# Performance work log

Measured on AMD Instinct MI355X. Metric: run time of the kernel, lower is better.

## Reference

```python
import jax, jax.numpy as jnp
import numpy as np

B, S, D, H = 8, 512, 1024, 16
DH = D // H
GAMMA = 0.1      # kl_gamma
KL_EPS = 1e-10
LN_EPS = 1e-5
SCALE = 1.0 / np.sqrt(DH).astype(np.float32)


def setup_inputs() -> dict:
    key = jax.random.key(0)
    ks = iter(jax.random.split(key, 32))
    rnd = lambda shape, s: jax.random.normal(next(ks), shape, jnp.float32) * s
    inp = {
        'title_features': rnd((B, S, D), 1.0),
        'content_features': rnd((B, S, D), 1.0),
    }
    for pre in ('t2c', 'c2t'):
        # small Q/K weights + bias 1.0 keep row-means of scores positive (log is defined)
        inp[pre + '_wq'] = rnd((D, D), 0.02); inp[pre + '_bq'] = jnp.ones((D,), jnp.float32)
        inp[pre + '_wk'] = rnd((D, D), 0.02); inp[pre + '_bk'] = jnp.ones((D,), jnp.float32)
        inp[pre + '_wv'] = rnd((D, D), 0.02); inp[pre + '_bv'] = jnp.zeros((D,), jnp.float32)
        inp[pre + '_wo'] = rnd((D, D), 0.02); inp[pre + '_bo'] = jnp.zeros((D,), jnp.float32)
    inp['gate_w'] = rnd((2 * D, D), 0.02)
    inp['gate_b'] = jnp.zeros((D,), jnp.float32)
    inp['ln_g'] = jnp.ones((D,), jnp.float32)
    inp['ln_b'] = jnpps = jnp.zeros((D,), jnp.float32)
    inp['ln_b'] = jnp.zeros((D,), jnp.float32)
    return inp


def _daa(q_in, k_in, v_in, wq, bq, wk, bk, wv, bv, wo, bo):
    """DivergenceAlignedAttention forward (eval mode, use_uniform_target=False)."""
    Bq, Sq, _ = q_in.shape
    Sk = k_in.shape[1]
    Q = (q_in @ wq + bq).reshape(Bq, Sq, H, DH)
    K = (k_in @ wk + bk).reshape(Bq, Sk, H, DH)
    V = (v_in @ wv + bv).reshape(Bq, Sk, H, DH)
    scores = jnp.einsum('bqhd,bkhd->bhqk', Q, K) * SCALE           # [B,H,Sq,Sk]
    tgt = jnp.mean(scores, axis=-1, keepdims=True)                 # row mean
    scores = scores + GAMMA * jnp.log(tgt + KL_EPS)                # fused KL term
    attn = jax.nn.softmax(scores, axis=-1)
    ctx = jnp.einsum('bhqk,bkhd->bqhd', attn, V).reshape(Bq, Sq, D)
    return ctx @ wo + bo


def _layer_norm(x, g, b):
    mu = jnp.mean(x, axis=-1, keepdims=True)
    var = jnp.mean(jnp.square(x - mu), axis=-1, keepdims=True)
    return g * (x - mu) / jnp.sqrt(var + LN_EPS) + b


def reference(title_features, content_features,
              t2c_wq, t2c_bq, t2c_wk, t2c_bk, t2c_wv, t2c_bv, t2c_wo, t2c_bo,
              c2t_wq, c2t_bq, c2t_wk, c2t_bk, c2t_wv, c2t_bv, c2t_wo, c2t_bo,
              gate_w, gate_b, ln_g, ln_b):
    t2c = _daa(content_features, title_features, title_features,
               t2c_wq, t2c_bq, t2c_wk, t2c_bk, t2c_wv, t2c_bv, t2c_wo, t2c_bo)
    c2t = _daa(title_features, content_features, content_features,
               c2t_wq, c2t_bq, c2t_wk, c2t_bk, c2t_wv, c2t_bv, c2t_wo, c2t_bo)
    gate_t = jax.nn.sigmoid(jnp.concatenate([title_features, t2c], axis=-1) @ gate_w + gate_b)
    gate_c = jax.nn.sigmoid(jnp.concatenate([content_features, c2t], axis=-1) @ gate_w + gate_b)
    fused_title = _layer_norm(gate_t * title_features + (1.0 - gate_t) * t2c, ln_g, ln_b)
    fused_content = _layer_norm(gate_c * content_features + (1.0 - gate_c) * c2t, ln_g, ln_b)
    return (fused_title, fused_content)
```

## Files before the change

### kernel.cpp

```cpp
#include <hip/hip_runtime.h>
#include <cstdint>
#include <cstddef>

typedef unsigned short ushort_t;
typedef unsigned int u32;
typedef __attribute__((ext_vector_type(8))) short bf16x8;
typedef __attribute__((ext_vector_type(4))) float f32x4;
typedef __attribute__((ext_vector_type(4))) unsigned short u16x4;

#define DEV static __device__ __forceinline__

DEV ushort_t f2bf(float f) {
  u32 x = __float_as_uint(f);
  x += 0x7fff + ((x >> 16) & 1);
  return (ushort_t)(x >> 16);
}
DEV float bf2f(ushort_t u) { return __uint_as_float(((u32)u) << 16); }

DEV void gload16(const ushort_t* g, ushort_t* l) {
  __builtin_amdgcn_global_load_lds(
      (const __attribute__((address_space(1))) void*)g,
      (__attribute__((address_space(3))) void*)l, 16, 0, 0);
}

#define VMW(n) asm volatile("s_waitcnt vmcnt(" #n ")" ::: "memory")
#define LGKM0 asm volatile("s_waitcnt lgkmcnt(0)" ::: "memory")
#define BAR() __builtin_amdgcn_s_barrier()


__global__ __launch_bounds__(256) void cvt_inputs(
    const float* __restrict__ xa, const float* __restrict__ xb,
    ushort_t* __restrict__ oa, ushort_t* __restrict__ ob) {
  int i = blockIdx.x * 256 + threadIdx.x;
  f32x4 va = ((const f32x4*)xa)[i];
  f32x4 vb = ((const f32x4*)xb)[i];
  u16x4 ua, ub;
#pragma unroll
  for (int j = 0; j < 4; ++j) { ua[j] = f2bf(va[j]); ub[j] = f2bf(vb[j]); }
  ((u16x4*)oa)[i] = ua;
  ((u16x4*)ob)[i] = ub;
}

struct Src11 { const float* p[11]; };

__global__ __launch_bounds__(256) void transpose_cvt(
    Src11 srcs, ushort_t* __restrict__ WTall, ushort_t* __restrict__ WgT,
    ushort_t* __restrict__ WoBF) {
  const int z = blockIdx.z;
  if (z != 8 && blockIdx.y >= 32) return;
  const float* src = srcs.p[z];
  int tx = threadIdx.x & 31, ty = threadIdx.x >> 5;
  int n0 = blockIdx.x << 5, k0 = blockIdx.y << 5;
  if (z >= 9) {
    ushort_t* dst = WoBF + ((size_t)(z - 9) << 20);
#pragma unroll
    for (int i = 0; i < 4; ++i) {
      size_t off = (size_t)(k0 + ty + i * 8) * 1024 + n0 + tx;
      dst[off] = f2bf(src[off]);
    }
    return;
  }
  const int K = (z == 8) ? 2048 : 1024;
  ushort_t* dst = (z == 8) ? WgT : WTall + ((size_t)z << 20);
  __shared__ float t[32][33];
#pragma unroll
  for (int i = 0; i < 4; ++i)
    t[ty + i * 8][tx] = src[(size_t)(k0 + ty + i * 8) * 1024 + n0 + tx];
  __syncthreads();
#pragma unroll
  for (int i = 0; i < 4; ++i)
    dst[(size_t)(n0 + ty + i * 8) * K + k0 + tx] = f2bf(t[tx][ty + i * 8]);
}

__global__ __launch_bounds__(256) void gb2_kernel(
    const float* __restrict__ bo0, const float* __restrict__ bo1,
    const ushort_t* __restrict__ WgT, float* __restrict__ gb2) {
  int idx = blockIdx.x * 256 + threadIdx.x;
  int dir = idx >> 10, n = idx & 1023;
  const float* bo = dir ? bo1 : bo0;
  const ushort_t* wrow = WgT + ((size_t)n << 11) + 1024;
  float s = 0.f;
  for (int k = 0; k < 1024; ++k) s += bo[k] * bf2f(wrow[k]);
  gb2[idx] = s;
}

__global__ __launch_bounds__(256, 3) void gemm_wp(
    const ushort_t* __restrict__ WgT, const ushort_t* __restrict__ WoBF,
    ushort_t* __restrict__ WpT) {
  __shared__ ushort_t As[128 * 64];
  __shared__ ushort_t Bs[128 * 64];
  const int tid = threadIdx.x;
  const int w = tid >> 6, lane = tid & 63;
  const int g = lane >> 4, c = lane & 15;
  const int wm = (w >> 1) << 6, wn = (w & 1) << 6;
  const int m0 = blockIdx.x << 7, n0 = blockIdx.y << 7;
  const int group = m0 >> 10;
  const int csw = (lane & 7) ^ (lane >> 3);

  f32x4 acc[4][4];
#pragma unroll
  for (int i = 0; i < 4; ++i)
#pragma unroll
    for (int j = 0; j < 4; ++j) acc[i][j] = f32x4{0.f, 0.f, 0.f, 0.f};

  for (int k0 = 0; k0 < 1024; k0 += 64) {
#pragma unroll
    for (int i = 0; i < 4; ++i) {
      const int chunk = (w << 2) + i;
      const int row = (chunk << 3) + (lane >> 3);
      gload16(WgT + ((size_t)((m0 + row) & 1023) << 11) + 1024 + k0 + (csw << 3),
              &As[(size_t)chunk << 9]);
      gload16(WoBF + ((size_t)group << 20) + ((size_t)(n0 + row) << 10) + k0 + (csw << 3),
              &Bs[(size_t)chunk << 9]);
    }
    __syncthreads();
    const int cg = c & 7;
#pragma unroll
    for (int ks = 0; ks < 2; ++ks) {
      bf16x8 af[4], bfr[4];
#pragma unroll
      for (int mi = 0; mi < 4; ++mi)
        af[mi] = *(const bf16x8*)&As[((wm + mi * 16 + c) << 6) +
                                     ((((ks << 2) | g) ^ cg) << 3)];
#pragma unroll
      for (int ni = 0; ni < 4; ++ni)
        bfr[ni] = *(const bf16x8*)&Bs[((wn + ni * 16 + c) << 6) +
                                      ((((ks << 2) | g) ^ cg) << 3)];
#pragma unroll
      for (int mi = 0; mi < 4; ++mi)
#pragma unroll
        for (int ni = 0; ni < 4; ++ni)
          acc[mi][ni] = __builtin_amdgcn_mfma_f32_16x16x32_bf16(
              af[mi], bfr[ni], acc[mi][ni], 0, 0, 0);
    }
    __syncthreads();
  }
#pragma unroll
  for (int ni = 0; ni < 4; ++ni) {
    const int n = n0 + wn + ni * 16 + c;
#pragma unroll
    for (int mi = 0; mi < 4; ++mi) {
      const int mb = m0 + wm + mi * 16 + (g << 2);
      f32x4 a = acc[mi][ni];
#pragma unroll
      for (int r = 0; r < 4; ++r)
        WpT[((size_t)group << 20) + ((size_t)((mb + r) & 1023) << 10) + n] = f2bf(a[r]);
    }
  }
}

enum { G_QKV = 0, G_OG = 1 };
struct Bias8 { const float* p[8]; };

#define RD_A(Q)                                                                \
  _Pragma("unroll") for (int m2 = 0; m2 < 2; ++m2)                             \
    _Pragma("unroll") for (int kk = 0; kk < 2; ++kk)                           \
      af[m2][kk] = *(const bf16x8*)&As[buf][(((wm << 7) + (((Q)*2 + m2) << 4) + c) << 6) + \
                                           ((((kk << 2) | g) ^ c7) << 3)]
#define MM(Q)                                                                  \
  _Pragma("unroll") for (int m2 = 0; m2 < 2; ++m2)                             \
    _Pragma("unroll") for (int nf = 0; nf < 4; ++nf) {                         \
      acc[(Q)*2 + m2][nf] = __builtin_amdgcn_mfma_f32_16x16x32_bf16(           \
          af[m2][0], bfr[nf][0], acc[(Q)*2 + m2][nf], 0, 0, 0);                \
      acc[(Q)*2 + m2][nf] = __builtin_amdgcn_mfma_f32_16x16x32_bf16(           \
          af[m2][1], bfr[nf][1], acc[(Q)*2 + m2][nf], 0, 0, 0);                \
    }

#define GTILE(T_, ST_, V0_, V1_, V2_, V3_)                                     \
  do {                                                                         \
    const int buf = (T_)&1;                                                    \
    const int ko = ((T_) + 1) << 6;                                            \
    bf16x8 af[2][2];                                                           \
    VMW(V0_); BAR();                                                           \
    _Pragma("unroll") for (int nf = 0; nf < 4; ++nf)                           \
      _Pragma("unroll") for (int kk = 0; kk < 2; ++kk)                         \
        bfr[nf][kk] = *(const bf16x8*)&Bs[buf][(((wn << 6) + (nf << 4) + c) << 6) + \
                                              ((((kk << 2) | g) ^ c7) << 3)];  \
    RD_A(0);                                                                   \
    if (ST_) stageB(buf ^ 1, ko, 0);                                           \
    BAR(); LGKM0;                                                              \
    __builtin_amdgcn_s_setprio(1); MM(0); __builtin_amdgcn_s_setprio(0);       \
    VMW(V1_); BAR();                                                           \
    RD_A(1);                                                                   \
    if (ST_) stageB(buf ^ 1, ko, 1);                                           \
    BAR(); LGKM0;                                                              \
    __builtin_amdgcn_s_setprio(1); MM(1); __builtin_amdgcn_s_setprio(0);       \
    VMW(V2_); BAR();                                                           \
    RD_A(2);                                                                   \
    if (ST_) { stageA(buf ^ 1, ko, 0); stageA(buf ^ 1, ko, 1); }               \
    BAR(); LGKM0;                                                              \
    __builtin_amdgcn_s_setprio(1); MM(2); __builtin_amdgcn_s_setprio(0);       \
    VMW(V3_); BAR();                                                           \
    RD_A(3);                                                                   \
    if (ST_) { stageA(buf ^ 1, ko, 2); stageA(buf ^ 1, ko, 3); }               \
    BAR(); LGKM0;                                                              \
    __builtin_amdgcn_s_setprio(1); MM(3); __builtin_amdgcn_s_setprio(0);       \
  } while (0)

template <int MODE>
__global__ __launch_bounds__(512, 2) void gemm256(
    const ushort_t* __restrict__ Aa, const ushort_t* __restrict__ Ab,
    const ushort_t* __restrict__ WTall, const ushort_t* __restrict__ WgT,
    const ushort_t* __restrict__ WpT, Bias8 bt,
    ushort_t* __restrict__ outQ, ushort_t* __restrict__ gl) {
  __shared__ ushort_t As[2][16384];
  __shared__ ushort_t Bs[2][16384];
  const int tid = threadIdx.x;
  const int wid = tid >> 6, lane = tid & 63;
  const int g = lane >> 4, c = lane & 15, c7 = c & 7;
  const int wm = wid >> 2, wn = wid & 3;
  constexpr int NB = (MODE == G_QKV) ? 512 : 256;
  const int bid = (int)blockIdx.x;
  const int wk = (bid & 7) * (NB >> 3) + (bid >> 3);
  const int mt = wk & 31, nt = wk >> 5;
  const int m0 = mt << 8, n0 = nt << 8;
  const int group = m0 >> 12;
  const int nch = n0 >> 10;

  const ushort_t* Asrc = (MODE == G_QKV)
      ? (group ? Ab : Aa) + ((size_t)(m0 & 4095) << 10)
      : Aa + ((size_t)m0 << 10);

  const ushort_t* Bbase;
  int bstride, bidx = -1;
  if (MODE == G_QKV) {
    if (nch < 3) {
      bidx = group * 3 + nch;
      Bbase = WTall + ((size_t)bidx << 20) + ((size_t)(n0 & 1023) << 10);
      bstride = 1024;
    } else {
      Bbase = WgT + ((size_t)(n0 & 1023) << 11);
      bstride = 2048;
    }
  } else {
    if (nch == 0) {
      Bbase = WTall + ((size_t)(6 + group) << 20) + ((size_t)n0 << 10);
      bstride = 1024;
    } else {
      Bbase = WpT + ((size_t)group << 20) + ((size_t)(n0 & 1023) << 10);
      bstride = 1024;
    }
  }

  auto stageB = [&](int bf_, int ko, int h) {
#pragma unroll
    for (int i = 0; i < 2; ++i) {
      int rl = (i << 6) + (wid << 3) + (lane >> 3);
      int row = (h << 7) + rl;
      int cs = (lane & 7) ^ (lane >> 3);
      gload16(Bbase + (size_t)row * bstride + ko + (cs << 3),
              &Bs[bf_][(h << 13) + (i << 12) + (wid << 9)]);
    }
  };
  auto stageA = [&](int bf_, int ko, int q) {
    int rl = (wid << 3) + (lane >> 3);
    int row = (q << 5) + (rl & 31) + ((rl & 32) << 2);
    int cs = (lane & 7) ^ (lane >> 3);
    gload16(Asrc + ((size_t)row << 10) + ko + (cs << 3),
            &As[bf_][((q << 5) + ((wid & 3) << 3) + ((wid >> 2) << 7)) << 6]);
  };

  f32x4 acc[8][4];
#pragma unroll
  for (int i = 0; i < 8; ++i)
#pragma unroll
    for (int j = 0; j < 4; ++j) acc[i][j] = f32x4{0.f, 0.f, 0.f, 0.f};

  stageB(0, 0, 0); stageB(0, 0, 1);
  stageA(0, 0, 0); stageA(0, 0, 1); stageA(0, 0, 2); stageA(0, 0, 3);

  bf16x8 bfr[4][2];
  for (int t = 0; t < 15; ++t) GTILE(t, 1, 3, 4, 5, 6);
  GTILE(15, 0, 3, 2, 1, 0);

  const float* bp_ = (MODE == G_QKV) ? (nch < 3 ? bt.p[bidx] : bt.p[6])
                                     : (nch == 0 ? bt.p[group] : bt.p[2 + group]);
#pragma unroll
  for (int mf = 0; mf < 8; ++mf) {
    const int mb = m0 + (wm << 7) + (mf << 4) + (g << 2);
#pragma unroll
    for (int nf = 0; nf < 4; ++nf) {
      const int n = n0 + (wn << 6) + (nf << 4) + c;
      const int nloc = n & 1023;
      const float bv = bp_[nloc];
      f32x4 a = acc[mf][nf];
      if (MODE == G_QKV) {
        if (nch < 3) {
          const int mrow = mb & 4095, b = mrow >> 9, s = mrow & 511;
          const int h = nloc >> 6, d = nloc & 63;
          ushort_t* base = outQ + ((size_t)bidx << 22);
          if (bidx == 1 || bidx == 5) {
            u16x4 o;
#pragma unroll
            for (int r = 0; r < 4; ++r) o[r] = f2bf(a[r] + bv);
            *(u16x4*)&base[(((size_t)((b * 16 + h) * 64 + d)) << 9) + s] = o;
          } else {
#pragma unroll
            for (int r = 0; r < 4; ++r)
              base[(((size_t)((b * 16 + h) * 512 + s + r)) << 6) + d] = f2bf(a[r] + bv);
          }
        } else {
#pragma unroll
          for (int r = 0; r < 4; ++r)
            gl[((size_t)(mb + r) << 10) + nloc] = f2bf(a[r] + bv);
        }
      } else {
        if (nch == 0) {
#pragma unroll
          for (int r = 0; r < 4; ++r)
            outQ[((size_t)(mb + r) << 10) + nloc] = f2bf(a[r] + bv);
        } else {
#pragma unroll
          for (int r = 0; r < 4; ++r) {
            size_t off = ((size_t)(mb + r) << 10) + nloc;
            gl[off] = f2bf(a[r] + bv + bf2f(gl[off]));
          }
        }
      }
    }
  }
}

__global__ __launch_bounds__(256, 2) void attn_kernel(
    const ushort_t* __restrict__ QKV, ushort_t* __restrict__ ctx) {
  __shared__ ushort_t kv[2][8192];
  const int tid = threadIdx.x, w = tid >> 6, lane = tid & 63;
  const int g = lane >> 4, c = lane & 15, c7 = c & 7;
  const int bid = (int)blockIdx.x;
  const int wid = (bid & 7) * 256 + (bid >> 3);
  const int dir = wid >> 10;
  const int bh = (wid >> 3) & 127, qt = wid & 7;
  const int q0 = (qt << 6) + (w << 4);
  const int qs = dir ? 2 : 3, ks = dir ? 4 : 0, vs = dir ? 5 : 1;
  const ushort_t* Qb = QKV + ((size_t)qs << 22) + ((size_t)bh << 15);
  const ushort_t* Kb = QKV + ((size_t)ks << 22) + ((size_t)bh << 15);
  const ushort_t* Vb = QKV + ((size_t)vs << 22) + ((size_t)bh << 15);

  auto stageK = [&](int b, int kc) {
#pragma unroll
    for (int i = 0; i < 4; ++i) {
      int idx = tid + (i << 8);
      int r = idx >> 3, sl = idx & 7;
      int cs = sl ^ (r & 7);
      gload16(Kb + (((size_t)((kc << 7) + r)) << 6) + (cs << 3), &kv[b][idx << 3]);
    }
  };
  auto stageV = [&](int b, int vc) {
#pragma unroll
    for (int i = 0; i < 4; ++i) {
      int idx = tid + (i << 8);
      int r = idx >> 4, sl = idx & 15;
      int cs = sl ^ (r & 15);
      gload16(Vb + ((size_t)r << 9) + (vc << 7) + (cs << 3), &kv[b][idx << 3]);
    }
  };

  bf16x8 qf0 = *(const bf16x8*)&Qb[((q0 + c) << 6) + (g << 3)];
  bf16x8 qf1 = *(const bf16x8*)&Qb[((q0 + c) << 6) + 32 + (g << 3)];

  f32x4 s[32];
  float mx = -1e30f;
  int buf = 0;
  stageK(0, 0);
  __syncthreads();
#pragma unroll
  for (int kc = 0; kc < 4; ++kc) {
    if (kc < 3) stageK(buf ^ 1, kc + 1);
    __builtin_amdgcn_s_setprio(1);
#pragma unroll
    for (int t = 0; t < 8; ++t) {
      const ushort_t* base = &kv[buf][((t << 4) + c) << 6];
      bf16x8 a0 = *(const bf16x8*)&base[(g ^ c7) << 3];
      bf16x8 a1 = *(const bf16x8*)&base[((4 | g) ^ c7) << 3];
      f32x4 z = {0.f, 0.f, 0.f, 0.f};
      z = __builtin_amdgcn_mfma_f32_16x16x32_bf16(a0, qf0, z, 0, 0, 0);
      z = __builtin_amdgcn_mfma_f32_16x16x32_bf16(a1, qf1, z, 0, 0, 0);
      s[kc * 8 + t] = z;
      mx = fmaxf(mx, fmaxf(fmaxf(z[0], z[1]), fmaxf(z[2], z[3])));
    }
    __builtin_amdgcn_s_setprio(0);
    __syncthreads();
    buf ^= 1;
  }
  stageV(0, 0);
  buf = 0;

  mx = fmaxf(mx, __shfl_xor(mx, 16, 64));
  mx = fmaxf(mx, __shfl_xor(mx, 32, 64));
  const float SC = 0.125f;
  float sum = 0.f;
#pragma unroll
  for (int t = 0; t < 32; ++t) {
#pragma unroll
    for (int r = 0; r < 4; ++r) {
      float p = __expf((s[t][r] - mx) * SC);
      s[t][r] = p;
      sum += p;
    }
  }
  sum += __shfl_xor(sum, 16, 64);
  sum += __shfl_xor(sum, 32, 64);
  const float inv = 1.0f / sum;

  f32x4 pacc[4];
#pragma unroll
  for (int dt = 0; dt < 4; ++dt) pacc[dt] = f32x4{0.f, 0.f, 0.f, 0.f};
  const int s1 = ((g & 1) << 5) + c;
  const int s2 = s1 + 16;
  const bool hi = (g >> 1) != 0;
  __syncthreads();
#pragma unroll
  for (int vc = 0; vc < 4; ++vc) {
    if (vc < 3) stageV(buf ^ 1, vc + 1);
#pragma unroll
    for (int t2l = 0; t2l < 4; ++t2l) {
      const int t2 = (vc << 2) + t2l;
      u32 A0 = ((u32)f2bf(s[2 * t2][1]) << 16) | f2bf(s[2 * t2][0]);
      u32 A1p = ((u32)f2bf(s[2 * t2][3]) << 16) | f2bf(s[2 * t2][2]);
      u32 B0 = ((u32)f2bf(s[2 * t2 + 1][1]) << 16) | f2bf(s[2 * t2 + 1][0]);
      u32 B1 = ((u32)f2bf(s[2 * t2 + 1][3]) << 16) | f2bf(s[2 * t2 + 1][2]);
      u32 xA0 = (u32)__shfl((int)A0, s1, 64), xA1 = (u32)__shfl((int)A1p, s1, 64);
      u32 xB0 = (u32)__shfl((int)B0, s1, 64), xB1 = (u32)__shfl((int)B1, s1, 64);
      u32 yA0 = (u32)__shfl((int)A0, s2, 64), yA1 = (u32)__shfl((int)A1p, s2, 64);
      u32 yB0 = (u32)__shfl((int)B0, s2, 64), yB1 = (u32)__shfl((int)B1, s2, 64);
      union { bf16x8 v; u32 wd[4]; } pb;
      pb.wd[0] = hi ? xB0 : xA0;
      pb.wd[1] = hi ? xB1 : xA1;
      pb.wd[2] = hi ? yB0 : yA0;
      pb.wd[3] = hi ? yB1 : yA1;
      __builtin_amdgcn_s_setprio(1);
#pragma unroll
      for (int dt = 0; dt < 4; ++dt) {
        bf16x8 av = *(const bf16x8*)
            &kv[buf][(((dt << 4) + c) << 7) + ((((t2l << 2) | g) ^ c) << 3)];
        pacc[dt] = __builtin_amdgcn_mfma_f32_16x16x32_bf16(av, pb.v, pacc[dt], 0, 0, 0);
      }
      __builtin_amdgcn_s_setprio(0);
    }
    __syncthreads();
    buf ^= 1;
  }

  const int b = bh >> 4, h = bh & 15;
  size_t obase = ((size_t)dir << 22) + ((size_t)(b * 512 + q0 + c) << 10) + (h << 6);
#pragma unroll
  for (int dt = 0; dt < 4; ++dt) {
    u16x4 o;
#pragma unroll
    for (int r = 0; r < 4; ++r) o[r] = f2bf(pacc[dt][r] * inv);
    *(u16x4*)&ctx[obase + (dt << 4) + (g << 2)] = o;
  }
}

__global__ __launch_bounds__(256) void fuse_ln(
    const float* __restrict__ xt, const float* __restrict__ xc,
    const ushort_t* __restrict__ ao, const ushort_t* __restrict__ gl,
    const float* __restrict__ lng, const float* __restrict__ lnb,
    float* __restrict__ out) {
  const int row = blockIdx.x, dir = row >> 12, r = row & 4095;
  const float* x = (dir ? xc : xt) + ((size_t)r << 10);
  const ushort_t* a = ao + ((size_t)row << 10);
  const ushort_t* glr = gl + ((size_t)row << 10);
  float* o = out + ((size_t)row << 10);
  const int t = threadIdx.x, w = t >> 6, lane = t & 63;
  f32x4 xv = ((const f32x4*)x)[t];
  u16x4 av = ((const u16x4*)a)[t];
  u16x4 gv = ((const u16x4*)glr)[t];
  f32x4 f;
  float sm = 0.f, sq = 0.f;
#pragma unroll
  for (int j = 0; j < 4; ++j) {
    float gate = 1.f / (1.f + __expf(-bf2f(gv[j])));
    float fv = gate * xv[j] + (1.f - gate) * bf2f(av[j]);
    f[j] = fv; sm += fv; sq += fv * fv;
  }
#pragma unroll
  for (int d = 1; d < 64; d <<= 1) {
    sm += __shfl_xor(sm, d, 64);
    sq += __shfl_xor(sq, d, 64);
  }
  __shared__ float ps[8];
  if (lane == 0) { ps[w] = sm; ps[4 + w] = sq; }
  __syncthreads();
  sm = ps[0] + ps[1] + ps[2] + ps[3];
  sq = ps[4] + ps[5] + ps[6] + ps[7];
  const float mu = sm * (1.f / 1024.f);
  const float var = sq * (1.f / 1024.f) - mu * mu;
  const float rstd = rsqrtf(var + 1e-5f);
  f32x4 lg = ((const f32x4*)lng)[t], lb = ((const f32x4*)lnb)[t];
  f32x4 ov;
#pragma unroll
  for (int j = 0; j < 4; ++j) ov[j] = lg[j] * (f[j] - mu) * rstd + lb[j];
  ((f32x4*)o)[t] = ov;
}

extern "C" void kernel_launch(void* const* d_in, const int* in_sizes, int n_in,
                              void* d_out, int out_size, void* d_ws, size_t ws_size,
                              hipStream_t stream) {
  (void)in_sizes; (void)n_in; (void)out_size; (void)ws_size;
  const float* title = (const float*)d_in[0];
  const float* content = (const float*)d_in[1];

  char* ws = (char*)d_ws;
  const size_t MB = 1u << 20;
  ushort_t* Xt    = (ushort_t*)(ws + 0 * MB);
  ushort_t* Xc    = (ushort_t*)(ws + 8 * MB);
  ushort_t* ctx   = (ushort_t*)(ws + 0 * MB);
  ushort_t* WTall = (ushort_t*)(ws + 16 * MB);
  ushort_t* WgT   = (ushort_t*)(ws + 32 * MB);
  ushort_t* QKV   = (ushort_t*)(ws + 36 * MB);
  ushort_t* ao    = (ushort_t*)(ws + 36 * MB);
  ushort_t* gl    = (ushort_t*)(ws + 84 * MB);
  ushort_t* WoBF  = (ushort_t*)(ws + 100 * MB);
  ushort_t* WpT   = (ushort_t*)(ws + 104 * MB);
  float*    gb2   = (float*)   (ws + 108 * MB);

  cvt_inputs<<<4096, 256, 0, stream>>>(title, content, Xt, Xc);

  Src11 srcs;
  srcs.p[0] = (const float*)d_in[4];  srcs.p[1] = (const float*)d_in[6];
  srcs.p[2] = (const float*)d_in[10]; srcs.p[3] = (const float*)d_in[2];
  srcs.p[4] = (const float*)d_in[12]; srcs.p[5] = (const float*)d_in[14];
  srcs.p[6] = (const float*)d_in[8];  srcs.p[7] = (const float*)d_in[16];
  srcs.p[8] = (const float*)d_in[18];
  srcs.p[9] = (const float*)d_in[8];  srcs.p[10] = (const float*)d_in[16];
  transpose_cvt<<<dim3(32, 64, 11), 256, 0, stream>>>(srcs, WTall, WgT, WoBF);

  gb2_kernel<<<8, 256, 0, stream>>>((const float*)d_in[9], (const float*)d_in[17],
                                    WgT, gb2);
  gemm_wp<<<dim3(16, 8), 256, 0, stream>>>(WgT, WoBF, WpT);

  Bias8 bq;
  bq.p[0] = (const float*)d_in[5];  bq.p[1] = (const float*)d_in[7];
  bq.p[2] = (const float*)d_in[11]; bq.p[3] = (const float*)d_in[3];
  bq.p[4] = (const float*)d_in[13]; bq.p[5] = (const float*)d_in[15];
  bq.p[6] = (const float*)d_in[19]; bq.p[7] = nullptr;
  gemm256<G_QKV><<<512, 512, 0, stream>>>(Xt, Xc, WTall, WgT, WpT, bq, QKV, gl);

  attn_kernel<<<2048, 256, 0, stream>>>(QKV, ctx);

  Bias8 bo;
  bo.p[0] = (const float*)d_in[9]; bo.p[1] = (const float*)d_in[17];
  bo.p[2] = gb2; bo.p[3] = gb2 + 1024;
  for (int i = 4; i < 8; ++i) bo.p[i] = nullptr;
  gemm256<G_OG><<<256, 512, 0, stream>>>(ctx, nullptr, WTall, WgT, WpT, bo, ao, gl);

  fuse_ln<<<8192, 256, 0, stream>>>(title, content, ao, gl,
                                    (const float*)d_in[20], (const float*)d_in[21],
                                    (float*)d_out);
}
```

Baseline: 253.2 us.

## Replace 256x256 pipelined GEMM with simpler 128x128 tiles and split gate partials

Swaps the 512-thread, 256x256-tile, double-buffered GEMM with a 256-thread, 128x128-tile, single-buffered kernel that runs more blocks per CU. The gate projection no longer does a read-modify-write on a shared buffer: the QKV pass writes the title/content gate part (with its bias and folded bo term) and the output pass writes its partial to a separate buffer. fuse_ln then sums the two partials before the sigmoid. The gb2 bias kernel also moves from one thread per output to one wave per output with a shuffle reduction. The trade is more tiles and no software pipelining inside the GEMM in exchange for higher occupancy and no read-after-write on gl, at the cost of one extra buffer read in fuse_ln.

```diff
diff --git a/kernel.cpp b/kernel.cpp
--- a/kernel.cpp
+++ b/kernel.cpp
@@ -22,10 +22,6 @@
       (const __attribute__((address_space(1))) void*)g,
       (__attribute__((address_space(3))) void*)l, 16, 0, 0);
 }
-
-#define VMW(n) asm volatile("s_waitcnt vmcnt(" #n ")" ::: "memory")
-#define LGKM0 asm volatile("s_waitcnt lgkmcnt(0)" ::: "memory")
-#define BAR() __builtin_amdgcn_s_barrier()
 
 
 __global__ __launch_bounds__(256) void cvt_inputs(
@@ -75,13 +71,17 @@
 __global__ __launch_bounds__(256) void gb2_kernel(
     const float* __restrict__ bo0, const float* __restrict__ bo1,
     const ushort_t* __restrict__ WgT, float* __restrict__ gb2) {
-  int idx = blockIdx.x * 256 + threadIdx.x;
-  int dir = idx >> 10, n = idx & 1023;
+  const int wgl = blockIdx.x * 4 + (threadIdx.x >> 6);
+  const int lane = threadIdx.x & 63;
+  const int dir = wgl >> 10, n = wgl & 1023;
   const float* bo = dir ? bo1 : bo0;
-  const ushort_t* wrow = WgT + ((size_t)n << 11) + 1024;
+  const ushort_t* wrow = WgT + ((size_t)n << 11) + 1024 + (lane << 4);
   float s = 0.f;
-  for (int k = 0; k < 1024; ++k) s += bo[k] * bf2f(wrow[k]);
-  gb2[idx] = s;
+#pragma unroll
+  for (int j = 0; j < 16; ++j) s += bo[(lane << 4) + j] * bf2f(wrow[j]);
+#pragma unroll
+  for (int d = 1; d < 64; d <<= 1) s += __shfl_xor(s, d, 64);
+  if (lane == 0) gb2[wgl] = s;
 }
 
 __global__ __launch_bounds__(256, 3) void gemm_wp(
@@ -149,142 +149,106 @@
   }
 }
 
-enum { G_QKV = 0, G_OG = 1 };
+enum { M_QKVG = 0, M_OG = 1 };
 struct Bias8 { const float* p[8]; };
 
-#define RD_A(Q)                                                                \
-  _Pragma("unroll") for (int m2 = 0; m2 < 2; ++m2)                             \
-    _Pragma("unroll") for (int kk = 0; kk < 2; ++kk)                           \
-      af[m2][kk] = *(const bf16x8*)&As[buf][(((wm << 7) + (((Q)*2 + m2) << 4) + c) << 6) + \
-                                           ((((kk << 2) | g) ^ c7) << 3)]
-#define MM(Q)                                                                  \
-  _Pragma("unroll") for (int m2 = 0; m2 < 2; ++m2)                             \
-    _Pragma("unroll") for (int nf = 0; nf < 4; ++nf) {                         \
-      acc[(Q)*2 + m2][nf] = __builtin_amdgcn_mfma_f32_16x16x32_bf16(           \
-          af[m2][0], bfr[nf][0], acc[(Q)*2 + m2][nf], 0, 0, 0);                \
-      acc[(Q)*2 + m2][nf] = __builtin_amdgcn_mfma_f32_16x16x32_bf16(           \
-          af[m2][1], bfr[nf][1], acc[(Q)*2 + m2][nf], 0, 0, 0);                \
-    }
-
-#define GTILE(T_, ST_, V0_, V1_, V2_, V3_)                                     \
-  do {                                                                         \
-    const int buf = (T_)&1;                                                    \
-    const int ko = ((T_) + 1) << 6;                                            \
-    bf16x8 af[2][2];                                                           \
-    VMW(V0_); BAR();                                                           \
-    _Pragma("unroll") for (int nf = 0; nf < 4; ++nf)                           \
-      _Pragma("unroll") for (int kk = 0; kk < 2; ++kk)                         \
-        bfr[nf][kk] = *(const bf16x8*)&Bs[buf][(((wn << 6) + (nf << 4) + c) << 6) + \
-                                              ((((kk << 2) | g) ^ c7) << 3)];  \
-    RD_A(0);                                                                   \
-    if (ST_) stageB(buf ^ 1, ko, 0);                                           \
-    BAR(); LGKM0;                                                              \
-    __builtin_amdgcn_s_setprio(1); MM(0); __builtin_amdgcn_s_setprio(0);       \
-    VMW(V1_); BAR();                                                           \
-    RD_A(1);                                                                   \
-    if (ST_) stageB(buf ^ 1, ko, 1);                                           \
-    BAR(); LGKM0;                                                              \
-    __builtin_amdgcn_s_setprio(1); MM(1); __builtin_amdgcn_s_setprio(0);       \
-    VMW(V2_); BAR();                                                           \
-    RD_A(2);                                                                   \
-    if (ST_) { stageA(buf ^ 1, ko, 0); stageA(buf ^ 1, ko, 1); }               \
-    BAR(); LGKM0;                                                              \
-    __builtin_amdgcn_s_setprio(1); MM(2); __builtin_amdgcn_s_setprio(0);       \
-    VMW(V3_); BAR();                                                           \
-    RD_A(3);                                                                   \
-    if (ST_) { stageA(buf ^ 1, ko, 2); stageA(buf ^ 1, ko, 3); }               \
-    BAR(); LGKM0;                                                              \
-    __builtin_amdgcn_s_setprio(1); MM(3); __builtin_amdgcn_s_setprio(0);       \
-  } while (0)
-
 template <int MODE>
-__global__ __launch_bounds__(512, 2) void gemm256(
+__global__ __launch_bounds__(256, 3) void gemm_kernel(
     const ushort_t* __restrict__ Aa, const ushort_t* __restrict__ Ab,
     const ushort_t* __restrict__ WTall, const ushort_t* __restrict__ WgT,
-    const ushort_t* __restrict__ WpT, Bias8 bt,
-    ushort_t* __restrict__ outQ, ushort_t* __restrict__ gl) {
-  __shared__ ushort_t As[2][16384];
-  __shared__ ushort_t Bs[2][16384];
+    const ushort_t* __restrict__ WpT, Bias8 bt, const float* __restrict__ gb2,
+    ushort_t* __restrict__ outQ, ushort_t* __restrict__ gt) {
+  __shared__ ushort_t As[128 * 64];
+  __shared__ ushort_t Bs[128 * 64];
   const int tid = threadIdx.x;
-  const int wid = tid >> 6, lane = tid & 63;
-  const int g = lane >> 4, c = lane & 15, c7 = c & 7;
-  const int wm = wid >> 2, wn = wid & 3;
-  constexpr int NB = (MODE == G_QKV) ? 512 : 256;
+  const int w = tid >> 6, lane = tid & 63;
+  const int g = lane >> 4, c = lane & 15;
+  const int wm = (w >> 1) << 6, wn = (w & 1) << 6;
   const int bid = (int)blockIdx.x;
-  const int wk = (bid & 7) * (NB >> 3) + (bid >> 3);
-  const int mt = wk & 31, nt = wk >> 5;
-  const int m0 = mt << 8, n0 = nt << 8;
+  const int xcd = bid & 7, idx = bid >> 3;
+  const int mt = (xcd << 3) + (idx & 7), nt = idx >> 3;
+  const int m0 = mt << 7, n0 = nt << 7;
   const int group = m0 >> 12;
   const int nch = n0 >> 10;
-
-  const ushort_t* Asrc = (MODE == G_QKV)
-      ? (group ? Ab : Aa) + ((size_t)(m0 & 4095) << 10)
-      : Aa + ((size_t)m0 << 10);
-
-  const ushort_t* Bbase;
-  int bstride, bidx = -1;
-  if (MODE == G_QKV) {
+  const int csw = (lane & 7) ^ (lane >> 3);
+
+  const ushort_t* Asrc = (MODE == M_QKVG)
+      ? ((group ? Ab : Aa) + ((size_t)(m0 & 4095) << 10))
+      : (Aa + ((size_t)m0 << 10));
+
+  const ushort_t* Bb;
+  int bstr, bidx = -1;
+  if (MODE == M_QKVG) {
     if (nch < 3) {
       bidx = group * 3 + nch;
-      Bbase = WTall + ((size_t)bidx << 20) + ((size_t)(n0 & 1023) << 10);
-      bstride = 1024;
+      Bb = WTall + ((size_t)bidx << 20) + ((size_t)(n0 & 1023) << 10);
+      bstr = 1024;
     } else {
-      Bbase = WgT + ((size_t)(n0 & 1023) << 11);
-      bstride = 2048;
+      Bb = WgT + ((size_t)(n0 & 1023) << 11);
+      bstr = 2048;
     }
   } else {
     if (nch == 0) {
-      Bbase = WTall + ((size_t)(6 + group) << 20) + ((size_t)n0 << 10);
-      bstride = 1024;
+      Bb = WTall + ((size_t)(6 + group) << 20) + ((size_t)n0 << 10);
+      bstr = 1024;
     } else {
-      Bbase = WpT + ((size_t)group << 20) + ((size_t)(n0 & 1023) << 10);
-      bstride = 1024;
-    }
-  }
-
-  auto stageB = [&](int bf_, int ko, int h) {
-#pragma unroll
-    for (int i = 0; i < 2; ++i) {
-      int rl = (i << 6) + (wid << 3) + (lane >> 3);
-      int row = (h << 7) + rl;
-      int cs = (lane & 7) ^ (lane >> 3);
-      gload16(Bbase + (size_t)row * bstride + ko + (cs << 3),
-              &Bs[bf_][(h << 13) + (i << 12) + (wid << 9)]);
-    }
-  };
-  auto stageA = [&](int bf_, int ko, int q) {
-    int rl = (wid << 3) + (lane >> 3);
-    int row = (q << 5) + (rl & 31) + ((rl & 32) << 2);
-    int cs = (lane & 7) ^ (lane >> 3);
-    gload16(Asrc + ((size_t)row << 10) + ko + (cs << 3),
-            &As[bf_][((q << 5) + ((wid & 3) << 3) + ((wid >> 2) << 7)) << 6]);
-  };
-
-  f32x4 acc[8][4];
-#pragma unroll
-  for (int i = 0; i < 8; ++i)
+      Bb = WpT + ((size_t)group << 20) + ((size_t)(n0 & 1023) << 10);
+      bstr = 1024;
+    }
+  }
+
+  f32x4 acc[4][4];
+#pragma unroll
+  for (int i = 0; i < 4; ++i)
 #pragma unroll
     for (int j = 0; j < 4; ++j) acc[i][j] = f32x4{0.f, 0.f, 0.f, 0.f};
 
-  stageB(0, 0, 0); stageB(0, 0, 1);
-  stageA(0, 0, 0); stageA(0, 0, 1); stageA(0, 0, 2); stageA(0, 0, 3);
-
-  bf16x8 bfr[4][2];
-  for (int t = 0; t < 15; ++t) GTILE(t, 1, 3, 4, 5, 6);
-  GTILE(15, 0, 3, 2, 1, 0);
-
-  const float* bp_ = (MODE == G_QKV) ? (nch < 3 ? bt.p[bidx] : bt.p[6])
-                                     : (nch == 0 ? bt.p[group] : bt.p[2 + group]);
-#pragma unroll
-  for (int mf = 0; mf < 8; ++mf) {
-    const int mb = m0 + (wm << 7) + (mf << 4) + (g << 2);
-#pragma unroll
-    for (int nf = 0; nf < 4; ++nf) {
-      const int n = n0 + (wn << 6) + (nf << 4) + c;
-      const int nloc = n & 1023;
-      const float bv = bp_[nloc];
-      f32x4 a = acc[mf][nf];
-      if (MODE == G_QKV) {
+  for (int k0 = 0; k0 < 1024; k0 += 64) {
+#pragma unroll
+    for (int i = 0; i < 4; ++i) {
+      const int chunk = (w << 2) + i;
+      const int row = (chunk << 3) + (lane >> 3);
+      gload16(Asrc + ((size_t)row << 10) + k0 + (csw << 3), &As[(size_t)chunk << 9]);
+      gload16(Bb + (size_t)row * bstr + k0 + (csw << 3), &Bs[(size_t)chunk << 9]);
+    }
+    __syncthreads();
+    const int cg = c & 7;
+#pragma unroll
+    for (int ks = 0; ks < 2; ++ks) {
+      bf16x8 af[4], bfr[4];
+#pragma unroll
+      for (int mi = 0; mi < 4; ++mi)
+        af[mi] = *(const bf16x8*)&As[((wm + mi * 16 + c) << 6) +
+                                     ((((ks << 2) | g) ^ cg) << 3)];
+#pragma unroll
+      for (int ni = 0; ni < 4; ++ni)
+        bfr[ni] = *(const bf16x8*)&Bs[((wn + ni * 16 + c) << 6) +
+                                      ((((ks << 2) | g) ^ cg) << 3)];
+#pragma unroll
+      for (int mi = 0; mi < 4; ++mi)
+#pragma unroll
+        for (int ni = 0; ni < 4; ++ni)
+          acc[mi][ni] = __builtin_amdgcn_mfma_f32_16x16x32_bf16(
+              af[mi], bfr[ni], acc[mi][ni], 0, 0, 0);
+    }
+    __syncthreads();
+  }
+
+#pragma unroll
+  for (int ni = 0; ni < 4; ++ni) {
+    const int n = n0 + wn + ni * 16 + c;
+    const int nloc = n & 1023;
+    float bv;
+    if (MODE == M_QKVG)
+      bv = (nch < 3) ? bt.p[bidx][nloc]
+                     : bt.p[6][nloc] + gb2[(group << 10) + nloc];
+    else
+      bv = (nch == 0) ? bt.p[group][nloc] : 0.f;
+#pragma unroll
+    for (int mi = 0; mi < 4; ++mi) {
+      const int mb = m0 + wm + mi * 16 + (g << 2);
+      f32x4 a = acc[mi][ni];
+      if (MODE == M_QKVG) {
         if (nch < 3) {
           const int mrow = mb & 4095, b = mrow >> 9, s = mrow & 511;
           const int h = nloc >> 6, d = nloc & 63;
@@ -302,7 +266,7 @@
         } else {
 #pragma unroll
           for (int r = 0; r < 4; ++r)
-            gl[((size_t)(mb + r) << 10) + nloc] = f2bf(a[r] + bv);
+            gt[((size_t)(mb + r) << 10) + nloc] = f2bf(a[r] + bv);
         }
       } else {
         if (nch == 0) {
@@ -311,10 +275,8 @@
             outQ[((size_t)(mb + r) << 10) + nloc] = f2bf(a[r] + bv);
         } else {
 #pragma unroll
-          for (int r = 0; r < 4; ++r) {
-            size_t off = ((size_t)(mb + r) << 10) + nloc;
-            gl[off] = f2bf(a[r] + bv + bf2f(gl[off]));
-          }
+          for (int r = 0; r < 4; ++r)
+            gt[((size_t)(mb + r) << 10) + nloc] = f2bf(a[r]);
         }
       }
     }
@@ -454,23 +416,26 @@
 
 __global__ __launch_bounds__(256) void fuse_ln(
     const float* __restrict__ xt, const float* __restrict__ xc,
-    const ushort_t* __restrict__ ao, const ushort_t* __restrict__ gl,
+    const ushort_t* __restrict__ ao, const ushort_t* __restrict__ gt,
+    const ushort_t* __restrict__ gp,
     const float* __restrict__ lng, const float* __restrict__ lnb,
     float* __restrict__ out) {
   const int row = blockIdx.x, dir = row >> 12, r = row & 4095;
   const float* x = (dir ? xc : xt) + ((size_t)r << 10);
   const ushort_t* a = ao + ((size_t)row << 10);
-  const ushort_t* glr = gl + ((size_t)row << 10);
+  const ushort_t* g1 = gt + ((size_t)row << 10);
+  const ushort_t* g2 = gp + ((size_t)row << 10);
   float* o = out + ((size_t)row << 10);
   const int t = threadIdx.x, w = t >> 6, lane = t & 63;
   f32x4 xv = ((const f32x4*)x)[t];
   u16x4 av = ((const u16x4*)a)[t];
-  u16x4 gv = ((const u16x4*)glr)[t];
+  u16x4 gv = ((const u16x4*)g1)[t];
+  u16x4 pv = ((const u16x4*)g2)[t];
   f32x4 f;
   float sm = 0.f, sq = 0.f;
 #pragma unroll
   for (int j = 0; j < 4; ++j) {
-    float gate = 1.f / (1.f + __expf(-bf2f(gv[j])));
+    float gate = 1.f / (1.f + __expf(-(bf2f(gv[j]) + bf2f(pv[j]))));
     float fv = gate * xv[j] + (1.f - gate) * bf2f(av[j]);
     f[j] = fv; sm += fv; sq += fv * fv;
   }
@@ -510,7 +475,8 @@
   ushort_t* WgT   = (ushort_t*)(ws + 32 * MB);
   ushort_t* QKV   = (ushort_t*)(ws + 36 * MB);
   ushort_t* ao    = (ushort_t*)(ws + 36 * MB);
-  ushort_t* gl    = (ushort_t*)(ws + 84 * MB);
+  ushort_t* gpart = (ushort_t*)(ws + 52 * MB);
+  ushort_t* gt    = (ushort_t*)(ws + 84 * MB);
   ushort_t* WoBF  = (ushort_t*)(ws + 100 * MB);
   ushort_t* WpT   = (ushort_t*)(ws + 104 * MB);
   float*    gb2   = (float*)   (ws + 108 * MB);
@@ -526,8 +492,8 @@
   srcs.p[9] = (const float*)d_in[8];  srcs.p[10] = (const float*)d_in[16];
   transpose_cvt<<<dim3(32, 64, 11), 256, 0, stream>>>(srcs, WTall, WgT, WoBF);
 
-  gb2_kernel<<<8, 256, 0, stream>>>((const float*)d_in[9], (const float*)d_in[17],
-                                    WgT, gb2);
+  gb2_kernel<<<512, 256, 0, stream>>>((const float*)d_in[9], (const float*)d_in[17],
+                                      WgT, gb2);
   gemm_wp<<<dim3(16, 8), 256, 0, stream>>>(WgT, WoBF, WpT);
 
   Bias8 bq;
@@ -535,17 +501,18 @@
   bq.p[2] = (const float*)d_in[11]; bq.p[3] = (const float*)d_in[3];
   bq.p[4] = (const float*)d_in[13]; bq.p[5] = (const float*)d_in[15];
   bq.p[6] = (const float*)d_in[19]; bq.p[7] = nullptr;
-  gemm256<G_QKV><<<512, 512, 0, stream>>>(Xt, Xc, WTall, WgT, WpT, bq, QKV, gl);
+  gemm_kernel<M_QKVG><<<2048, 256, 0, stream>>>(Xt, Xc, WTall, WgT, WpT, bq, gb2,
+                                                QKV, gt);
 
   attn_kernel<<<2048, 256, 0, stream>>>(QKV, ctx);
 
   Bias8 bo;
   bo.p[0] = (const float*)d_in[9]; bo.p[1] = (const float*)d_in[17];
-  bo.p[2] = gb2; bo.p[3] = gb2 + 1024;
-  for (int i = 4; i < 8; ++i) bo.p[i] = nullptr;
-  gemm256<G_OG><<<256, 512, 0, stream>>>(ctx, nullptr, WTall, WgT, WpT, bo, ao, gl);
-
-  fuse_ln<<<8192, 256, 0, stream>>>(title, content, ao, gl,
+  for (int i = 2; i < 8; ++i) bo.p[i] = nullptr;
+  gemm_kernel<M_OG><<<1024, 256, 0, stream>>>(ctx, nullptr, WTall, WgT, WpT, bo, gb2,
+                                              ao, gpart);
+
+  fuse_ln<<<8192, 256, 0, stream>>>(title, content, ao, gt, gpart,
                                     (const float*)d_in[20], (const float*)d_in[21],
                                     (float*)d_out);
 }
```

Result: faster. 226.4 us (-10.6%).
